# Kernel tuning notes

Measured on AMD Instinct MI355X. Metric: run time of the kernel, lower is better.

The kernel has to match this reference:

```python
import jax, jax.numpy as jnp
import numpy as np

B, K, D, LS, NL = 32, 64, 256, 128, 2


def _xavier(key, shape):
    # torch xavier_uniform for Linear weight [out, in]
    fan_out, fan_in = shape[-2], shape[-1]
    lim = float(np.sqrt(6.0 / (fan_in + fan_out)))
    return jax.random.uniform(key, shape, jnp.float32, -lim, lim)


def setup_inputs():
    key = jax.random.key(0)
    ks = jax.random.split(key, 32)
    inp = {
        "X": jax.random.normal(ks[0], (B, K, D), jnp.float32),
        # per-layer stacked params [NL, ...]
        "k_w": _xavier(ks[1], (NL, D, D)),
        "q_w": _xavier(ks[2], (NL, D, D)),
        "rv_w1": _xavier(ks[3], (NL, D, 2 * D)),
        "rv_b1": jnp.zeros((NL, D), jnp.float32),
        "rv_w2": _xavier(ks[4], (NL, D, D)),
        "rv_b2": jnp.zeros((NL, D), jnp.float32),
        "ln_g": jnp.ones((NL, D), jnp.float32),
        "ln_b": jnp.zeros((NL, D), jnp.float32),
        "mlp_w1": _xavier(ks[5], (NL, D, D)),
        "mlp_b1": jnp.zeros((NL, D), jnp.float32),
        "mlp_w2": _xavier(ks[6], (NL, D, D)),
        "mlp_b2": jnp.zeros((NL, D), jnp.float32),
        "proj_w": _xavier(ks[7], (LS, D)),
        "proj_b": jnp.zeros((LS,), jnp.float32),
        "mu_w": _xavier(ks[8], (LS, LS)),
        "mu_b": jnp.zeros((LS,), jnp.float32),
        "sp_w": _xavier(ks[9], (LS, LS)),
        "sp_b": jnp.zeros((LS,), jnp.float32),
    }
    return inp


def _gelu(x):
    return jax.nn.gelu(x, approximate=False)


def _layernorm(x, g, b, eps=1e-5):
    m = jnp.mean(x, axis=-1, keepdims=True)
    v = jnp.mean((x - m) ** 2, axis=-1, keepdims=True)
    return (x - m) / jnp.sqrt(v + eps) * g + b


def _block(x, kw, qw, rw1, rb1, rw2, rb2, lg, lb, mw1, mb1, mw2, mb2):
    scale = D ** (-0.5)
    x_orig = x
    # pairwise difference r[b,i,j,:] = x[b,i]-x[b,j]
    r = x[:, :, None, :] - x[:, None, :, :]                      # [B,K,K,D]
    xi = jnp.broadcast_to(x[:, :, None, :], (B, K, K, D))
    cat = jnp.concatenate([xi, r], axis=-1)                      # [B,K,K,2D]
    v = _gelu(jnp.einsum('bijc,dc->bijd', cat, rw1) + rb1)
    v = jnp.einsum('bijd,ed->bije', v, rw2) + rb2                # [B,K,K,D]
    k = jnp.einsum('bid,ed->bie', x, kw)
    q = jnp.einsum('bid,ed->bie', x, qw) * scale
    attn = jax.nn.softmax(jnp.einsum('bid,bjd->bij', q, k), axis=2)
    agg = jnp.einsum('bij,bijd->bid', attn, v)
    h = _layernorm(x_orig + agg, lg, lb)
    h = jnp.einsum('bid,ed->bie', _gelu(jnp.einsum('bid,ed->bie', h, mw1) + mb1), mw2) + mb2
    return x_orig + h


def reference(X, k_w, q_w, rv_w1, rv_b1, rv_w2, rv_b2, ln_g, ln_b,
              mlp_w1, mlp_b1, mlp_w2, mlp_b2, proj_w, proj_b,
              mu_w, mu_b, sp_w, sp_b):
    x = X
    for i in range(NL):
        x = _block(x, k_w[i], q_w[i], rv_w1[i], rv_b1[i], rv_w2[i], rv_b2[i],
                   ln_g[i], ln_b[i], mlp_w1[i], mlp_b1[i], mlp_w2[i], mlp_b2[i])
    s = jnp.sum(x, axis=1)                                        # [B,D]
    h = _gelu(s @ proj_w.T + proj_b)                              # [B,LS]
    mu = h @ mu_w.T + mu_b
    scale = jax.nn.softplus(h @ sp_w.T + sp_b)
    return (mu, scale)
```

## Files before the change

### kernel.cpp

```cpp
#include <hip/hip_runtime.h>
#include <hip/hip_bf16.h>


using bf16 = __hip_bfloat16;
typedef short bf16x8 __attribute__((ext_vector_type(8)));
typedef float f32x4 __attribute__((ext_vector_type(4)));

__device__ __forceinline__ float bfu(unsigned short u) { return __uint_as_float(((unsigned)u) << 16); }

__device__ __forceinline__ unsigned short bfr(float v) {
  unsigned u = __float_as_uint(v);
  u += 0x7FFFu + ((u >> 16) & 1u);
  return (unsigned short)(u >> 16);
}

__device__ __forceinline__ float gelu_e(float x) {
  return 0.5f * x * (1.0f + erff(x * 0.7071067811865475f));
}

__device__ __forceinline__ float load_f(const void* p, int i, int fl) {
  if (fl) return bfu(((const unsigned short*)p)[i]);
  return ((const float*)p)[i];
}

__device__ __forceinline__ int block_detect(const void* X) {
  __shared__ int bad_s;
  if (threadIdx.x == 0) bad_s = 0;
  __syncthreads();
  if (threadIdx.x < 256) {
    const float v = bfu(((const unsigned short*)X)[threadIdx.x]);
    if (!(fabsf(v) < 1e6f)) atomicOr(&bad_s, 1);
  }
  __syncthreads();
  return bad_s ? 0 : 1;
}

__device__ __forceinline__ void stage_split4(unsigned short (&aF)[2][4096], int row, int d0, float4 v) {
  ushort4 h, lo;
  h.x = bfr(v.x); h.y = bfr(v.y); h.z = bfr(v.z); h.w = bfr(v.w);
  lo.x = bfr(v.x - bfu(h.x)); lo.y = bfr(v.y - bfu(h.y));
  lo.z = bfr(v.z - bfu(h.z)); lo.w = bfr(v.w - bfu(h.w));
  const int kt = d0 >> 5, lane = row | (((d0 >> 3) & 3) << 4), j = d0 & 7;
  *(ushort4*)&aF[0][kt*512 + lane*8 + j] = h;
  *(ushort4*)&aF[1][kt*512 + lane*8 + j] = lo;
}

__global__ __launch_bounds__(256) void prep_kernel(
    const void* __restrict__ X, const void* __restrict__ kw, const void* __restrict__ qw,
    const void* __restrict__ rw1, const void* __restrict__ rw2, const void* __restrict__ mw1,
    const void* __restrict__ mw2, const void* __restrict__ pw, const void* __restrict__ muw,
    const void* __restrict__ spw,
    const void* __restrict__ rb1, const void* __restrict__ rb2, const void* __restrict__ lng,
    const void* __restrict__ lnb, const void* __restrict__ mb1, const void* __restrict__ mb2,
    const void* __restrict__ pb, const void* __restrict__ mub, const void* __restrict__ spb,
    unsigned short* __restrict__ wfb, unsigned short* __restrict__ w3b,
    float* __restrict__ wh, float* __restrict__ bc)
{
  __shared__ __align__(16) char psm[65536];
  const int fl = block_detect(X);
  const int t = threadIdx.x;
  int blk = blockIdx.x;

  if (blk < 16) {
    unsigned short* ls = (unsigned short*)psm;
    unsigned* lsu = (unsigned*)psm;
    const int l = blk >> 3, kt = blk & 7;
    if (fl) {
      #pragma unroll
      for (int s = 0; s < 4; ++s) {
        const unsigned* sp = (const unsigned*)((s == 0) ? kw : (s == 1) ? qw : rw1);
        const int rstr = (s < 2) ? 128 : 256;
        const int coff = ((s == 3) ? 128 : 0) + kt*16;
        for (int i = t; i < 4096; i += 256) {
          const int e = i >> 4, d2 = i & 15;
          lsu[s*4096 + i] = sp[(l*256 + e)*rstr + coff + d2];
        }
      }
    } else {
      #pragma unroll
      for (int s = 0; s < 4; ++s) {
        const float* sp = (const float*)((s == 0) ? kw : (s == 1) ? qw : rw1);
        const int rstr = (s < 2) ? 256 : 512;
        const int coff = ((s == 3) ? 256 : 0) + kt*32;
        for (int i = t; i < 4096; i += 256) {
          const int e = i >> 4, d2 = i & 15;
          const float f0 = sp[(l*256 + e)*rstr + coff + d2*2];
          const float f1 = sp[(l*256 + e)*rstr + coff + d2*2 + 1];
          lsu[s*4096 + i] = (unsigned)bfr(f0) | ((unsigned)bfr(f1) << 16);
        }
      }
    }
    __syncthreads();
    unsigned* outp = (unsigned*)wfb + (l*8 + kt)*16384;
    for (int f2 = t; f2 < 16384; f2 += 256) {
      const int j2 = f2 & 3, lane = (f2 >> 2) & 63, ntg = f2 >> 8;
      const int seg = ntg >> 4;
      const int e = (ntg & 15)*16 + (lane & 15);
      const int dl = ((lane >> 4) & 3)*8 + j2*2;
      unsigned short r0 = ls[seg*8192 + e*32 + dl];
      unsigned short r1 = ls[seg*8192 + e*32 + dl + 1];
      if (seg == 1) { r0 = bfr(bfu(r0)*0.0625f); r1 = bfr(bfu(r1)*0.0625f); }
      else if (seg == 2) {
        const unsigned short w0 = ls[3*8192 + e*32 + dl];
        const unsigned short w1 = ls[3*8192 + e*32 + dl + 1];
        r0 = bfr(bfu(r0) + bfu(w0)); r1 = bfr(bfu(r1) + bfu(w1));
      }
      outp[f2] = (unsigned)r0 | ((unsigned)r1 << 16);
    }
    return;
  }
  blk -= 16;
  if (blk < 48) {
    unsigned short* ls = (unsigned short*)psm;
    unsigned* lsu = (unsigned*)psm;
    const int l3 = blk >> 3, kt = blk & 7;
    const int l = l3 / 3, gm = l3 % 3;
    const void* src = (gm == 0) ? rw2 : (gm == 1) ? mw1 : mw2;
    if (fl) {
      const unsigned* sp = (const unsigned*)src;
      for (int i = t; i < 4096; i += 256) {
        const int e = i >> 4, d2 = i & 15;
        lsu[i] = sp[(l*256 + e)*128 + kt*16 + d2];
      }
    } else {
      const float* sp = (const float*)src;
      for (int i = t; i < 4096; i += 256) {
        const int e = i >> 4, d2 = i & 15;
        const float f0 = sp[(l*256 + e)*256 + kt*32 + d2*2];
        const float f1 = sp[(l*256 + e)*256 + kt*32 + d2*2 + 1];
        lsu[i] = (unsigned)bfr(f0) | ((unsigned)bfr(f1) << 16);
      }
    }
    __syncthreads();
    unsigned* outp = (unsigned*)w3b + (l3*8 + kt)*4096;
    for (int f2 = t; f2 < 4096; f2 += 256) {
      const int j2 = f2 & 3, lane = (f2 >> 2) & 63, nt = f2 >> 8;
      const int e = nt*16 + (lane & 15);
      const int dl = ((lane >> 4) & 3)*8 + j2*2;
      outp[f2] = (unsigned)ls[e*32 + dl] | ((unsigned)ls[e*32 + dl + 1] << 16);
    }
    return;
  }
  blk -= 48;
  if (blk < 24) {
    float* lsf = (float*)psm;
    if (blk < 8) {
      const int l0 = blk*16;
      if (fl) {
        const unsigned* sp = (const unsigned*)pw;
        for (int i = t; i < 2048; i += 256) {
          const int ll = i >> 7, d2 = i & 127;
          const unsigned u = sp[(l0 + ll)*128 + d2];
          lsf[ll*256 + d2*2]     = __uint_as_float(u << 16);
          lsf[ll*256 + d2*2 + 1] = __uint_as_float(u & 0xffff0000u);
        }
      } else {
        const float* sp = (const float*)pw;
        for (int i = t; i < 4096; i += 256) {
          const int ll = i >> 8, d = i & 255;
          lsf[ll*256 + d] = sp[(l0 + ll)*256 + d];
        }
      }
      __syncthreads();
      for (int i = t; i < 4096; i += 256) {
        const int d = i >> 4, ll = i & 15;
        wh[d*128 + l0 + ll] = lsf[ll*256 + d];
      }
    } else {
      const int grp2 = blk - 8;
      const int isSp = grp2 >> 3;
      const int l0 = (grp2 & 7)*16;
      const void* src = isSp ? spw : muw;
      const int off = isSp ? 49152 : 32768;
      if (fl) {
        const unsigned* sp = (const unsigned*)src;
        for (int i = t; i < 1024; i += 256) {
          const int ll = i >> 6, c2 = i & 63;
          const unsigned u = sp[(l0 + ll)*64 + c2];
          lsf[ll*128 + c2*2]     = __uint_as_float(u << 16);
          lsf[ll*128 + c2*2 + 1] = __uint_as_float(u & 0xffff0000u);
        }
      } else {
        const float* sp = (const float*)src;
        for (int i = t; i < 2048; i += 256) {
          const int ll = i >> 7, c = i & 127;
          lsf[ll*128 + c] = sp[(l0 + ll)*128 + c];
        }
      }
      __syncthreads();
      for (int i = t; i < 2048; i += 256) {
        const int c = i >> 4, ll = i & 15;
        wh[off + c*128 + l0 + ll] = lsf[ll*128 + c];
      }
    }
    return;
  }
  for (int i = t; i < 3456; i += 256) {
    const void* src; int off;
    if (i < 512)       { src = rb1; off = i; }
    else if (i < 1024) { src = rb2; off = i - 512; }
    else if (i < 1536) { src = lng; off = i - 1024; }
    else if (i < 2048) { src = lnb; off = i - 1536; }
    else if (i < 2560) { src = mb1; off = i - 2048; }
    else if (i < 3072) { src = mb2; off = i - 2560; }
    else if (i < 3200) { src = pb;  off = i - 3072; }
    else if (i < 3328) { src = mub; off = i - 3200; }
    else               { src = spb; off = i - 3328; }
    bc[i] = load_f(src, off, fl);
  }
}

template<bool SPLIT, int NTG>
__device__ __forceinline__ void k1_body(
    const unsigned short (&aF)[2][4096],
    const unsigned short* __restrict__ wfb, const float* __restrict__ bc,
    float* __restrict__ kq, float* __restrict__ Pf, unsigned* __restrict__ Qpk,
    int l, int row0, int ntg0, int t)
{
  const int w = t >> 6, l64 = t & 63;
  const int col = l64 & 15, quad = l64 >> 4;
  f32x4 acc[NTG];
  #pragma unroll
  for (int i = 0; i < NTG; ++i) acc[i] = (f32x4){0.f, 0.f, 0.f, 0.f};
  for (int kt = 0; kt < 8; ++kt) {
    const bf16x8 ah = *(const bf16x8*)&aF[0][kt*512 + l64*8];
    bf16x8 al;
    if (SPLIT) al = *(const bf16x8*)&aF[1][kt*512 + l64*8];
    #pragma unroll
    for (int i = 0; i < NTG; ++i) {
      const int ntg = ntg0 + w*NTG + i;
      const bf16x8 b = *(const bf16x8*)&wfb[((l*8 + kt)*64 + ntg)*512 + l64*8];
      acc[i] = __builtin_amdgcn_mfma_f32_16x16x32_bf16(ah, b, acc[i], 0, 0, 0);
      if (SPLIT) acc[i] = __builtin_amdgcn_mfma_f32_16x16x32_bf16(al, b, acc[i], 0, 0, 0);
    }
  }
  #pragma unroll
  for (int i = 0; i < NTG; ++i) {
    const int ntg = ntg0 + w*NTG + i;
    if (ntg < 32) {
      const int n = ntg*16 + col;
      #pragma unroll
      for (int r = 0; r < 4; ++r)
        kq[(size_t)(row0 + quad*4 + r)*512 + n] = acc[i][r];
    } else if (ntg < 48) {
      const int c = (ntg - 32)*16 + col;
      const float bias = bc[l*256 + c];
      #pragma unroll
      for (int r = 0; r < 4; ++r)
        Pf[(size_t)(row0 + quad*4 + r)*256 + c] = acc[i][r] + bias;
    } else {
      #pragma unroll
      for (int r = 0; r < 4; ++r) {
        const float v = acc[i][r];
        const float pv = __shfl_xor(v, 1, 64);
        if (!(col & 1)) {
          const unsigned uu = (unsigned)bfr(v) | ((unsigned)bfr(pv) << 16);
          Qpk[(size_t)(row0 + quad*4 + r)*128 + (ntg - 48)*8 + (col >> 1)] = uu;
        }
      }
    }
  }
}

template<bool SPLIT, int NRR>
__device__ __forceinline__ void k1_body16(
    const unsigned short (&aF)[2][4096],
    const unsigned short* __restrict__ wfb, const float* __restrict__ bc,
    float* __restrict__ kq, float* __restrict__ Pf, unsigned* __restrict__ Qpk,
    int l, int row0, int t)
{
  const int w = t >> 6, l64 = t & 63;
  const int col = l64 & 15, quad = l64 >> 4;
  f32x4 acc[4];
  #pragma unroll
  for (int i = 0; i < 4; ++i) acc[i] = (f32x4){0.f, 0.f, 0.f, 0.f};
  for (int kt = 0; kt < 8; ++kt) {
    const bf16x8 ah = *(const bf16x8*)&aF[0][kt*512 + l64*8];
    bf16x8 al;
    if (SPLIT) al = *(const bf16x8*)&aF[1][kt*512 + l64*8];
    #pragma unroll
    for (int i = 0; i < 4; ++i) {
      const int ntg = w*4 + i;
      const bf16x8 b = *(const bf16x8*)&wfb[((l*8 + kt)*64 + ntg)*512 + l64*8];
      acc[i] = __builtin_amdgcn_mfma_f32_16x16x32_bf16(ah, b, acc[i], 0, 0, 0);
      if (SPLIT) acc[i] = __builtin_amdgcn_mfma_f32_16x16x32_bf16(al, b, acc[i], 0, 0, 0);
    }
  }
  #pragma unroll
  for (int i = 0; i < 4; ++i) {
    const int ntg = w*4 + i;
    if (ntg < 32) {
      const int n = ntg*16 + col;
      #pragma unroll
      for (int r = 0; r < 4; ++r)
        if (NRR == 16 || quad*4 + r < NRR)
          kq[(size_t)(row0 + quad*4 + r)*512 + n] = acc[i][r];
    } else if (ntg < 48) {
      const int c = (ntg - 32)*16 + col;
      const float bias = bc[l*256 + c];
      #pragma unroll
      for (int r = 0; r < 4; ++r)
        if (NRR == 16 || quad*4 + r < NRR)
          Pf[(size_t)(row0 + quad*4 + r)*256 + c] = acc[i][r] + bias;
    } else {
      #pragma unroll
      for (int r = 0; r < 4; ++r) {
        const float v = acc[i][r];
        const float pv = __shfl_xor(v, 1, 64);
        if (!(col & 1) && (NRR == 16 || quad*4 + r < NRR)) {
          const unsigned uu = (unsigned)bfr(v) | ((unsigned)bfr(pv) << 16);
          Qpk[(size_t)(row0 + quad*4 + r)*128 + (ntg - 48)*8 + (col >> 1)] = uu;
        }
      }
    }
  }
}

__global__ __launch_bounds__(256) void k1l0(
    const void* __restrict__ X, const unsigned short* __restrict__ wfb,
    const float* __restrict__ bc, float* __restrict__ kq, float* __restrict__ Pf,
    unsigned* __restrict__ Qpk)
{
  const int fl = block_detect(X);
  __shared__ __align__(16) unsigned short aF[2][4096];
  const int t = threadIdx.x;
  const int mb = (int)blockIdx.x >> 2, nb4 = (int)blockIdx.x & 3;
  const int row0 = mb * 16, ntg0 = nb4 * 16;
  if (fl) {
    for (int i = t; i < 512; i += 256) {
      const int row = i >> 5, d0 = (i & 31) * 8;
      const uint4 u = *(const uint4*)((const unsigned*)X + (size_t)(row0 + row)*128 + (i & 31)*4);
      const int kt = d0 >> 5, lane = row | (((d0 >> 3) & 3) << 4);
      *(uint4*)&aF[0][kt*512 + lane*8] = u;
    }
  } else {
    for (int i = t; i < 1024; i += 256) {
      const int row = i >> 6, d0 = (i & 63) * 4;
      stage_split4(aF, row, d0, *(const float4*)((const float*)X + (size_t)(row0 + row)*256 + d0));
    }
  }
  __syncthreads();
  if (fl) k1_body<false, 4>(aF, wfb, bc, kq, Pf, Qpk, 0, row0, ntg0, t);
  else    k1_body<true,  4>(aF, wfb, bc, kq, Pf, Qpk, 0, row0, ntg0, t);
}

template<int NR>
__device__ __forceinline__ void attn_phase1k(
    const float* __restrict__ kq, const float* __restrict__ Pf,
    const unsigned* __restrict__ Qpk,
    int row0, int t, float* qg, float* scp, float* als,
    unsigned* Kst, unsigned* Qst)
{
  const int base = row0 & ~63;
  for (int i = t; i < NR*64; i += 1024) {
    const int il = i >> 6, d0 = (i & 63)*4;
    *(float4*)&qg[il*256 + d0] = *(const float4*)&kq[(size_t)(row0 + il)*512 + 256 + d0];
  }
  for (int i = t; i < 4096; i += 1024) {
    const int row = i >> 6, c4 = i & 63;
    const float4 v = *(const float4*)&kq[(size_t)(base + row)*512 + c4*4];
    Kst[row*132 + c4*2]     = (unsigned)bfr(v.x) | ((unsigned)bfr(v.y) << 16);
    Kst[row*132 + c4*2 + 1] = (unsigned)bfr(v.z) | ((unsigned)bfr(v.w) << 16);
  }
  for (int i = t; i < 2048; i += 1024) {
    const int row = i >> 5, c4 = i & 31;
    *(uint4*)&Qst[row*128 + c4*4] = *(const uint4*)&Qpk[(size_t)(base + row)*128 + c4*4];
  }
  __syncthreads();
  const int w = t >> 6, lane = t & 63;
  {
    const int jl = lane & 15, part = lane >> 4;
    const int j = (w & 3)*16 + jl;
    const int i0 = (w >> 2) * 2;
    const unsigned* kr = &Kst[j*132 + part*32];
    const float* q0p = &qg[i0*256 + part*64];
    const float* q1p = &qg[(i0+1)*256 + part*64];
    float s0 = 0.f, s1 = 0.f;
    #pragma unroll
    for (int d2 = 0; d2 < 32; d2 += 2) {
      const unsigned ka = kr[d2], kb = kr[d2 + 1];
      const float4 q0 = *(const float4*)&q0p[d2*2];
      const float4 q1 = *(const float4*)&q1p[d2*2];
      const float k0 = bfu((unsigned short)ka), k1 = bfu((unsigned short)(ka >> 16));
      const float k2 = bfu((unsigned short)kb), k3 = bfu((unsigned short)(kb >> 16));
      s0 = fmaf(k0, q0.x, s0); s0 = fmaf(k1, q0.y, s0);
      s0 = fmaf(k2, q0.z, s0); s0 = fmaf(k3, q0.w, s0);
      s1 = fmaf(k0, q1.x, s1); s1 = fmaf(k1, q1.y, s1);
      s1 = fmaf(k2, q1.z, s1); s1 = fmaf(k3, q1.w, s1);
    }
    s0 += __shfl_xor(s0, 16, 64); s0 += __shfl_xor(s0, 32, 64);
    s1 += __shfl_xor(s1, 16, 64); s1 += __shfl_xor(s1, 32, 64);
    if (part == 0) { scp[i0*64 + j] = s0; scp[(i0+1)*64 + j] = s1; }
  }
  __syncthreads();
  if (w < NR) {
    const int r = w;
    float s = scp[r*64 + lane];
    float m = s;
    #pragma unroll
    for (int off = 32; off; off >>= 1) m = fmaxf(m, __shfl_xor(m, off, 64));
    const float e = __expf(s - m);
    float ss = e;
    #pragma unroll
    for (int off = 32; off; off >>= 1) ss += __shfl_xor(ss, off, 64);
    als[r*64 + lane] = e / ss;
  }
  __syncthreads();
  {
    const int cp = t & 127, rb = t >> 7;
    const float2 P = *(const float2*)&Pf[(size_t)(row0 + rb)*256 + cp*2];
    const float A0 = -1.702f * P.x, A1 = -1.702f * P.y;
    float a0 = 0.f, a1 = 0.f;
    const unsigned* qp = &Qst[cp];
    const float* ap = &als[rb*64];
    #pragma unroll 4
    for (int j = 0; j < 64; ++j) {
      const unsigned u = qp[j*128];
      const float wgt = ap[j];
      const float q0 = __uint_as_float(u << 16);
      const float q1 = __uint_as_float(u & 0xffff0000u);
      const float s0 = __builtin_amdgcn_rcpf(1.f + __expf(fmaf(1.702f, q0, A0)));
      const float s1 = __builtin_amdgcn_rcpf(1.f + __expf(fmaf(1.702f, q1, A1)));
      a0 = fmaf(wgt * (P.x - q0), s0, a0);
      a1 = fmaf(wgt * (P.y - q1), s1, a1);
    }
    qg[rb*256 + cp*2]     = a0;
    qg[rb*256 + cp*2 + 1] = a1;
  }
  __syncthreads();
}

__device__ __forceinline__ f32x4 k4_gemm16(
    const unsigned short (&aF)[2][4096],
    const unsigned short* __restrict__ wg, int w, int l64)
{
  f32x4 acc = (f32x4){0.f, 0.f, 0.f, 0.f};
  for (int kt = 0; kt < 8; ++kt) {
    const bf16x8 ah = *(const bf16x8*)&aF[0][kt*512 + l64*8];
    const bf16x8 al = *(const bf16x8*)&aF[1][kt*512 + l64*8];
    const bf16x8 b = *(const bf16x8*)&wg[((kt*16 + w)*64 + l64)*8];
    acc = __builtin_amdgcn_mfma_f32_16x16x32_bf16(ah, b, acc, 0, 0, 0);
    acc = __builtin_amdgcn_mfma_f32_16x16x32_bf16(al, b, acc, 0, 0, 0);
  }
  return acc;
}

template<bool ADAPT, bool TAIL, int NR>
__device__ __forceinline__ void k4_core1k(
    const float* gl, const void* __restrict__ xin, int fl,
    float* __restrict__ xout, const unsigned short* __restrict__ wg,
    const float* __restrict__ bc, int l, int row0, int t, bool writeX,
    unsigned short (&aF)[2][4096], float* bufB, float (&mv)[16][2])
{
  const int w = t >> 6, l64 = t & 63;
  const int col = l64 & 15, quad = l64 >> 4;
  const int cn = w*16 + col;
  const float* rb2c = bc + 512  + l*256;
  const float* lngc = bc + 1024 + l*256;
  const float* lnbc = bc + 1536 + l*256;
  const float* mb1c = bc + 2048 + l*256;
  const float* mb2c = bc + 2560 + l*256;

  for (int i = t; i < NR*64; i += 1024) {
    const int row = i >> 6, d0 = (i & 63) * 4;
    stage_split4(aF, row, d0, *(const float4*)&gl[row*256 + d0]);
  }
  if (ADAPT && fl) {
    for (int c = t; c < NR*128; c += 1024) {
      const int row = c >> 7, dp = c & 127;
      const unsigned u = ((const unsigned*)xin)[(size_t)(row0 + row)*128 + dp];
      bufB[row*260 + dp*2]     = __uint_as_float(u << 16);
      bufB[row*260 + dp*2 + 1] = __uint_as_float(u & 0xffff0000u);
    }
  } else {
    for (int c = t; c < NR*64; c += 1024) {
      const int row = c >> 6, d0 = (c & 63) * 4;
      *(float4*)&bufB[row*260 + d0] = *(const float4*)((const float*)xin + (size_t)(row0 + row)*256 + d0);
    }
  }
  __syncthreads();
  float xtr[4];
  #pragma unroll
  for (int r = 0; r < 4; ++r) xtr[r] = bufB[(quad*4 + r)*260 + cn];
  __syncthreads();

  f32x4 acc = k4_gemm16(aF, wg, w, l64);
  #pragma unroll
  for (int r = 0; r < 4; ++r)
    bufB[(quad*4 + r)*260 + cn] = acc[r] + rb2c[cn] + xtr[r];
  __syncthreads();
  {
    const int row = t >> 5, part = t & 31;
    if (row < NR) {
      float s = 0.f, s2 = 0.f;
      #pragma unroll
      for (int kk = 0; kk < 8; ++kk) {
        const float v = bufB[row*260 + part + kk*32];
        s += v; s2 = fmaf(v, v, s2);
      }
      #pragma unroll
      for (int off = 16; off; off >>= 1) {
        s  += __shfl_xor(s, off, 32);
        s2 += __shfl_xor(s2, off, 32);
      }
      if (part == 0) {
        const float mu = s * (1.f/256.f);
        mv[row][0] = mu;
        mv[row][1] = rsqrtf(fmaf(-mu, mu, s2 * (1.f/256.f)) + 1e-5f);
      }
    }
  }
  __syncthreads();
  for (int i = t; i < NR*64; i += 1024) {
    const int row = i >> 6, d0 = (i & 63) * 4;
    float4 v = *(const float4*)&bufB[row*260 + d0];
    const float m = mv[row][0], iv = mv[row][1];
    v.x = (v.x - m)*iv*lngc[d0]   + lnbc[d0];
    v.y = (v.y - m)*iv*lngc[d0+1] + lnbc[d0+1];
    v.z = (v.z - m)*iv*lngc[d0+2] + lnbc[d0+2];
    v.w = (v.w - m)*iv*lngc[d0+3] + lnbc[d0+3];
    stage_split4(aF, row, d0, v);
  }
  __syncthreads();
  acc = k4_gemm16(aF, wg + 65536, w, l64);
  #pragma unroll
  for (int r = 0; r < 4; ++r)
    if (quad*4 + r < NR)
      bufB[(quad*4 + r)*260 + cn] = gelu_e(acc[r] + mb1c[cn]);
  __syncthreads();
  for (int i = t; i < NR*64; i += 1024) {
    const int row = i >> 6, d0 = (i & 63) * 4;
    stage_split4(aF, row, d0, *(const float4*)&bufB[row*260 + d0]);
  }
  __syncthreads();
  acc = k4_gemm16(aF, wg + 2*65536, w, l64);
  if (TAIL) {
    #pragma unroll
    for (int r = 0; r < 4; ++r)
      bufB[(quad*4 + r)*260 + cn] = acc[r] + mb2c[cn] + xtr[r];
    __syncthreads();
    for (int i = t; i < NR*64; i += 1024) {
      const int row = i >> 6, d0 = (i & 63) * 4;
      const float4 v = *(const float4*)&bufB[row*260 + d0];
      if (writeX) *(float4*)&xout[(size_t)(row0 + row)*256 + d0] = v;
      stage_split4(aF, row, d0, v);
    }
    __syncthreads();
  } else {
    #pragma unroll
    for (int r = 0; r < 4; ++r)
      if (quad*4 + r < NR)
        xout[(size_t)(row0 + quad*4 + r)*256 + cn] = acc[r] + mb2c[cn] + xtr[r];
  }
}

#define SM_QG    0
#define SM_SCP   8192
#define SM_ALS   10240
#define SM_UNION 12288
#define SM_QST   46080
#define SM_AF    12288
#define SM_BUFB  28672
#define SM_MV    45312
#define SM_TOTAL 78848

__device__ __forceinline__ int swz_row0(int bid) {
  const int xcd = bid & 7, j = bid >> 3;
  const int batch = (j & 3)*8 + xcd;
  const int rsub = j >> 2;
  return batch*64 + rsub*8;
}

__global__ __launch_bounds__(1024) void kA_attn_mix_kq(
    const unsigned short* __restrict__ w3b, const unsigned short* __restrict__ wfb,
    const float* __restrict__ bc, const void* __restrict__ X, float* __restrict__ x,
    const float* __restrict__ kq, const float* __restrict__ Pf,
    const unsigned* __restrict__ Qpk,
    float* __restrict__ kq1, float* __restrict__ Pf1, unsigned* __restrict__ Qpk1)
{
  const int fl = block_detect(X);
  __shared__ __align__(16) char sm[SM_TOTAL];
  float* qg  = (float*)(sm + SM_QG);
  float* scp = (float*)(sm + SM_SCP);
  float* als = (float*)(sm + SM_ALS);
  unsigned* Kst = (unsigned*)(sm + SM_UNION);
  unsigned* Qst = (unsigned*)(sm + SM_QST);
  unsigned short (&aF)[2][4096] = *reinterpret_cast<unsigned short (*)[2][4096]>(sm + SM_AF);
  float* bufB = (float*)(sm + SM_BUFB);
  float (&mv)[16][2] = *reinterpret_cast<float (*)[16][2]>(sm + SM_MV);
  const int t = threadIdx.x;
  const int row0 = swz_row0((int)blockIdx.x);
  attn_phase1k<8>(kq, Pf, Qpk, row0, t, qg, scp, als, Kst, Qst);
  k4_core1k<true, true, 8>(qg, X, fl, x, w3b, bc, 0, row0, t, true, aF, bufB, mv);
  k1_body16<true, 8>(aF, wfb, bc, kq1, Pf1, Qpk1, 1, row0, t);
}

__global__ __launch_bounds__(1024) void kB_attn_fin(
    const unsigned short* __restrict__ w3b, const float* __restrict__ bc,
    float* __restrict__ x, const float* __restrict__ kq1,
    const float* __restrict__ Pf1, const unsigned* __restrict__ Qpk1)
{
  __shared__ __align__(16) char sm[SM_TOTAL];
  float* qg  = (float*)(sm + SM_QG);
  float* scp = (float*)(sm + SM_SCP);
  float* als = (float*)(sm + SM_ALS);
  unsigned* Kst = (unsigned*)(sm + SM_UNION);
  unsigned* Qst = (unsigned*)(sm + SM_QST);
  unsigned short (&aF)[2][4096] = *reinterpret_cast<unsigned short (*)[2][4096]>(sm + SM_AF);
  float* bufB = (float*)(sm + SM_BUFB);
  float (&mv)[16][2] = *reinterpret_cast<float (*)[16][2]>(sm + SM_MV);
  const int t = threadIdx.x;
  const int row0 = swz_row0((int)blockIdx.x);
  attn_phase1k<8>(kq1, Pf1, Qpk1, row0, t, qg, scp, als, Kst, Qst);
  k4_core1k<false, false, 8>(qg, x, 0, x, w3b + 3*65536, bc, 1, row0, t, true, aF, bufB, mv);
}

__global__ __launch_bounds__(256) void k5_head(
    const float* __restrict__ x, const float* __restrict__ wh,
    const float* __restrict__ bc, const void* __restrict__ X,
    void* __restrict__ out)
{
  const int fl = block_detect(X);
  __shared__ float ss[256];
  __shared__ float hh[128];
  const int b = blockIdx.x, t = threadIdx.x;
  {
    const float* xp = x + (size_t)(b << 6)*256 + t;
    float s0 = 0.f, s1 = 0.f, s2 = 0.f, s3 = 0.f;
    for (int i = 0; i < 64; i += 4) {
      s0 += xp[(size_t)(i    )*256];
      s1 += xp[(size_t)(i + 1)*256];
      s2 += xp[(size_t)(i + 2)*256];
      s3 += xp[(size_t)(i + 3)*256];
    }
    ss[t] = (s0 + s1) + (s2 + s3);
  }
  __syncthreads();
  if (t < 128) {
    float acc = bc[3072 + t];
    const float* projT = wh;
    for (int d = 0; d < 256; ++d) acc = fmaf(ss[d], projT[d*128 + t], acc);
    hh[t] = gelu_e(acc);
  }
  __syncthreads();
  float v; int oidx;
  if (t < 128) {
    float acc = bc[3200 + t];
    const float* muT = wh + 32768;
    for (int c = 0; c < 128; ++c) acc = fmaf(hh[c], muT[c*128 + t], acc);
    v = acc; oidx = b*128 + t;
  } else {
    const int u = t - 128;
    float acc = bc[3328 + u];
    const float* spT = wh + 49152;
    for (int c = 0; c < 128; ++c) acc = fmaf(hh[c], spT[c*128 + u], acc);
    v = (acc > 20.f) ? acc : log1pf(__expf(acc));
    oidx = 4096 + b*128 + u;
  }
  if (fl) ((bf16*)out)[oidx] = __float2bfloat16(v);
  else    ((float*)out)[oidx] = v;
}

extern "C" void kernel_launch(void* const* d_in, const int* in_sizes, int n_in,
                              void* d_out, int out_size, void* d_ws, size_t ws_size,
                              hipStream_t stream)
{
  (void)in_sizes; (void)n_in; (void)out_size; (void)ws_size;
  float* ws    = (float*)d_ws;
  float* x     = ws + 16;
  float* kq    = x + 524288;
  float* Pf    = kq + 1048576;
  unsigned* Qpk = (unsigned*)(Pf + 524288);
  float* g     = (float*)(Qpk + 262144);
  unsigned short* wfb = (unsigned short*)(g + 524288);
  unsigned short* w3b = wfb + 524288;
  float* wh    = (float*)(w3b + 393216);
  float* bc    = wh + 65536;
  float* kq1   = bc + 4096;
  float* Pf1   = kq1 + 1048576;
  unsigned* Qpk1 = (unsigned*)(Pf1 + 524288);

  prep_kernel<<<dim3(89), dim3(256), 0, stream>>>(
      d_in[0], d_in[1], d_in[2], d_in[3], d_in[5], d_in[9], d_in[11],
      d_in[13], d_in[15], d_in[17],
      d_in[4], d_in[6], d_in[7], d_in[8], d_in[10], d_in[12],
      d_in[14], d_in[16], d_in[18],
      wfb, w3b, wh, bc);
  k1l0<<<dim3(512), dim3(256), 0, stream>>>(d_in[0], wfb, bc, kq, Pf, Qpk);
  kA_attn_mix_kq<<<dim3(256), dim3(1024), 0, stream>>>(
      w3b, wfb, bc, d_in[0], x, kq, Pf, Qpk, kq1, Pf1, Qpk1);
  kB_attn_fin<<<dim3(256), dim3(1024), 0, stream>>>(w3b, bc, x, kq1, Pf1, Qpk1);
  k5_head<<<dim3(32), dim3(256), 0, stream>>>(x, wh, bc, d_in[0], (void*)d_out);
}
```

Before: 187.2 us.

## Fuse attention kernels and head into one kernel with per-batch atomic barriers

Merges the layer-0 attention/mix kernel, the layer-1 attention kernel and the head kernel into a single launch. Blocks of the same batch synchronise through a spin-wait counter in workspace, and the last block to finish each batch (found with an atomic ticket) runs the head. The head's reductions are also split across 1024 threads. This removes two kernel launches and their gaps, at the cost of relying on all 8 blocks of a batch being co-resident for the spin barrier, plus spin and fence overhead.

Result: slower. 432.2 us (+130.9%).

```diff
diff --git a/kernel.cpp b/kernel.cpp
--- a/kernel.cpp
+++ b/kernel.cpp
@@ -54,7 +54,7 @@
     const void* __restrict__ lnb, const void* __restrict__ mb1, const void* __restrict__ mb2,
     const void* __restrict__ pb, const void* __restrict__ mub, const void* __restrict__ spb,
     unsigned short* __restrict__ wfb, unsigned short* __restrict__ w3b,
-    float* __restrict__ wh, float* __restrict__ bc)
+    float* __restrict__ wh, float* __restrict__ bc, unsigned* __restrict__ cnt)
 {
   __shared__ __align__(16) char psm[65536];
   const int fl = block_detect(X);
@@ -195,6 +195,7 @@
     }
     return;
   }
+  for (int i = t; i < 64; i += 256) cnt[i] = 0u;
   for (int i = t; i < 3456; i += 256) {
     const void* src; int off;
     if (i < 512)       { src = rb1; off = i; }
@@ -571,15 +572,18 @@
   return batch*64 + rsub*8;
 }
 
-__global__ __launch_bounds__(1024) void kA_attn_mix_kq(
+__global__ __launch_bounds__(1024) void kABh(
     const unsigned short* __restrict__ w3b, const unsigned short* __restrict__ wfb,
     const float* __restrict__ bc, const void* __restrict__ X, float* __restrict__ x,
     const float* __restrict__ kq, const float* __restrict__ Pf,
     const unsigned* __restrict__ Qpk,
-    float* __restrict__ kq1, float* __restrict__ Pf1, unsigned* __restrict__ Qpk1)
+    float* __restrict__ kq1, float* __restrict__ Pf1, unsigned* __restrict__ Qpk1,
+    const float* __restrict__ wh, void* __restrict__ out,
+    unsigned* __restrict__ cnt1, unsigned* __restrict__ cnt2)
 {
   const int fl = block_detect(X);
   __shared__ __align__(16) char sm[SM_TOTAL];
+  __shared__ unsigned rank_s;
   float* qg  = (float*)(sm + SM_QG);
   float* scp = (float*)(sm + SM_SCP);
   float* als = (float*)(sm + SM_ALS);
@@ -590,75 +594,87 @@
   float (&mv)[16][2] = *reinterpret_cast<float (*)[16][2]>(sm + SM_MV);
   const int t = threadIdx.x;
   const int row0 = swz_row0((int)blockIdx.x);
+  const int batch = row0 >> 6;
+
   attn_phase1k<8>(kq, Pf, Qpk, row0, t, qg, scp, als, Kst, Qst);
   k4_core1k<true, true, 8>(qg, X, fl, x, w3b, bc, 0, row0, t, true, aF, bufB, mv);
   k1_body16<true, 8>(aF, wfb, bc, kq1, Pf1, Qpk1, 1, row0, t);
-}
-
-__global__ __launch_bounds__(1024) void kB_attn_fin(
-    const unsigned short* __restrict__ w3b, const float* __restrict__ bc,
-    float* __restrict__ x, const float* __restrict__ kq1,
-    const float* __restrict__ Pf1, const unsigned* __restrict__ Qpk1)
-{
-  __shared__ __align__(16) char sm[SM_TOTAL];
-  float* qg  = (float*)(sm + SM_QG);
-  float* scp = (float*)(sm + SM_SCP);
-  float* als = (float*)(sm + SM_ALS);
-  unsigned* Kst = (unsigned*)(sm + SM_UNION);
-  unsigned* Qst = (unsigned*)(sm + SM_QST);
-  unsigned short (&aF)[2][4096] = *reinterpret_cast<unsigned short (*)[2][4096]>(sm + SM_AF);
-  float* bufB = (float*)(sm + SM_BUFB);
-  float (&mv)[16][2] = *reinterpret_cast<float (*)[16][2]>(sm + SM_MV);
-  const int t = threadIdx.x;
-  const int row0 = swz_row0((int)blockIdx.x);
+
+  __threadfence();
+  __syncthreads();
+  if (t == 0) {
+    __hip_atomic_fetch_add(&cnt1[batch], 1u, __ATOMIC_RELEASE, __HIP_MEMORY_SCOPE_AGENT);
+    while (__hip_atomic_load(&cnt1[batch], __ATOMIC_ACQUIRE, __HIP_MEMORY_SCOPE_AGENT) < 8u)
+      __builtin_amdgcn_s_sleep(4);
+  }
+  __syncthreads();
+  __threadfence();
+
   attn_phase1k<8>(kq1, Pf1, Qpk1, row0, t, qg, scp, als, Kst, Qst);
   k4_core1k<false, false, 8>(qg, x, 0, x, w3b + 3*65536, bc, 1, row0, t, true, aF, bufB, mv);
-}
-
-__global__ __launch_bounds__(256) void k5_head(
-    const float* __restrict__ x, const float* __restrict__ wh,
-    const float* __restrict__ bc, const void* __restrict__ X,
-    void* __restrict__ out)
-{
-  const int fl = block_detect(X);
-  __shared__ float ss[256];
-  __shared__ float hh[128];
-  const int b = blockIdx.x, t = threadIdx.x;
+
+  __threadfence();
+  __syncthreads();
+  if (t == 0)
+    rank_s = __hip_atomic_fetch_add(&cnt2[batch], 1u, __ATOMIC_ACQ_REL, __HIP_MEMORY_SCOPE_AGENT);
+  __syncthreads();
+  if (rank_s != 7u) return;
+  __threadfence();
+
+  float* ss4 = (float*)(sm);
+  float* ssf = (float*)(sm + 4096);
+  float* hh  = (float*)(sm + 5120);
+  float* red = (float*)(sm + 8192);
   {
-    const float* xp = x + (size_t)(b << 6)*256 + t;
+    const int col = t & 255, q = t >> 8;
+    const float* xp = x + (size_t)(batch*64 + q*16)*256 + col;
     float s0 = 0.f, s1 = 0.f, s2 = 0.f, s3 = 0.f;
-    for (int i = 0; i < 64; i += 4) {
+    for (int i = 0; i < 16; i += 4) {
       s0 += xp[(size_t)(i    )*256];
       s1 += xp[(size_t)(i + 1)*256];
       s2 += xp[(size_t)(i + 2)*256];
       s3 += xp[(size_t)(i + 3)*256];
     }
-    ss[t] = (s0 + s1) + (s2 + s3);
+    ss4[q*256 + col] = (s0 + s1) + (s2 + s3);
+  }
+  __syncthreads();
+  if (t < 256) ssf[t] = (ss4[t] + ss4[256 + t]) + (ss4[512 + t] + ss4[768 + t]);
+  __syncthreads();
+  {
+    const int o = t & 127, ch = t >> 7;
+    float acc = 0.f;
+    #pragma unroll 4
+    for (int d = ch*32; d < ch*32 + 32; ++d) acc = fmaf(ssf[d], wh[d*128 + o], acc);
+    red[t] = acc;
   }
   __syncthreads();
   if (t < 128) {
-    float acc = bc[3072 + t];
-    const float* projT = wh;
-    for (int d = 0; d < 256; ++d) acc = fmaf(ss[d], projT[d*128 + t], acc);
-    hh[t] = gelu_e(acc);
-  }
-  __syncthreads();
-  float v; int oidx;
-  if (t < 128) {
-    float acc = bc[3200 + t];
-    const float* muT = wh + 32768;
-    for (int c = 0; c < 128; ++c) acc = fmaf(hh[c], muT[c*128 + t], acc);
-    v = acc; oidx = b*128 + t;
-  } else {
-    const int u = t - 128;
-    float acc = bc[3328 + u];
-    const float* spT = wh + 49152;
-    for (int c = 0; c < 128; ++c) acc = fmaf(hh[c], spT[c*128 + u], acc);
-    v = (acc > 20.f) ? acc : log1pf(__expf(acc));
-    oidx = 4096 + b*128 + u;
-  }
-  if (fl) ((bf16*)out)[oidx] = __float2bfloat16(v);
-  else    ((float*)out)[oidx] = v;
+    float a = bc[3072 + t];
+    #pragma unroll
+    for (int ch = 0; ch < 8; ++ch) a += red[t + ch*128];
+    hh[t] = gelu_e(a);
+  }
+  __syncthreads();
+  {
+    const int o2 = t & 255, ch = t >> 8;
+    const int isSp = o2 >> 7, o = o2 & 127;
+    const float* W = wh + (isSp ? 49152 : 32768);
+    float acc = 0.f;
+    #pragma unroll 4
+    for (int c = ch*32; c < ch*32 + 32; ++c) acc = fmaf(hh[c], W[c*128 + o], acc);
+    red[t] = acc;
+  }
+  __syncthreads();
+  if (t < 256) {
+    const int isSp = t >> 7, o = t & 127;
+    const float a = ((red[t] + red[t + 256]) + (red[t + 512] + red[t + 768]))
+                    + bc[(isSp ? 3328 : 3200) + o];
+    float v; int oidx;
+    if (isSp == 0) { v = a; oidx = batch*128 + o; }
+    else { v = (a > 20.f) ? a : log1pf(__expf(a)); oidx = 4096 + batch*128 + o; }
+    if (fl) ((bf16*)out)[oidx] = __float2bfloat16(v);
+    else    ((float*)out)[oidx] = v;
+  }
 }
 
 extern "C" void kernel_launch(void* const* d_in, const int* in_sizes, int n_in,
@@ -667,7 +683,8 @@
 {
   (void)in_sizes; (void)n_in; (void)out_size; (void)ws_size;
   float* ws    = (float*)d_ws;
-  float* x     = ws + 16;
+  unsigned* cnt = (unsigned*)ws;
+  float* x     = ws + 128;
   float* kq    = x + 524288;
   float* Pf    = kq + 1048576;
   unsigned* Qpk = (unsigned*)(Pf + 524288);
@@ -685,10 +702,9 @@
       d_in[13], d_in[15], d_in[17],
       d_in[4], d_in[6], d_in[7], d_in[8], d_in[10], d_in[12],
       d_in[14], d_in[16], d_in[18],
-      wfb, w3b, wh, bc);
+      wfb, w3b, wh, bc, cnt);
   k1l0<<<dim3(512), dim3(256), 0, stream>>>(d_in[0], wfb, bc, kq, Pf, Qpk);
-  kA_attn_mix_kq<<<dim3(256), dim3(1024), 0, stream>>>(
-      w3b, wfb, bc, d_in[0], x, kq, Pf, Qpk, kq1, Pf1, Qpk1);
-  kB_attn_fin<<<dim3(256), dim3(1024), 0, stream>>>(w3b, bc, x, kq1, Pf1, Qpk1);
-  k5_head<<<dim3(32), dim3(256), 0, stream>>>(x, wh, bc, d_in[0], (void*)d_out);
-}
+  kABh<<<dim3(256), dim3(1024), 0, stream>>>(
+      w3b, wfb, bc, d_in[0], x, kq, Pf, Qpk, kq1, Pf1, Qpk1,
+      wh, (void*)d_out, cnt, cnt + 32);
+}
```

## Halve rows per attention block to double grid size and re-split layer-0 projection

Applied to the files above, without the earlier changes.

The two fused attention kernels now give each block 4 query rows instead of 8 and launch 512 blocks instead of 256, so the GPU's CUs get more blocks to spread across. The per-row score, softmax and relation-aggregation loops are simplified to one output per thread to match. The layer-0 projection kernel now uses 512-thread blocks that cover 8 rows and 32 column tiles each, and both projection paths share one generic body. The cost is that every block re-stages the full 64-row K and Q tiles for fewer rows, and half of each 16-row MFMA tile is wasted. The new launch-bound occupancy hints may also limit registers and cause spills.

Result: slower. 195.7 us (+4.5%).

```diff
diff --git a/kernel.cpp b/kernel.cpp
--- a/kernel.cpp
+++ b/kernel.cpp
@@ -210,64 +210,12 @@
   }
 }
 
-template<bool SPLIT, int NTG>
-__device__ __forceinline__ void k1_body(
+template<bool SPLIT, int NRR>
+__device__ __forceinline__ void k1_bodyN(
     const unsigned short (&aF)[2][4096],
     const unsigned short* __restrict__ wfb, const float* __restrict__ bc,
     float* __restrict__ kq, float* __restrict__ Pf, unsigned* __restrict__ Qpk,
     int l, int row0, int ntg0, int t)
-{
-  const int w = t >> 6, l64 = t & 63;
-  const int col = l64 & 15, quad = l64 >> 4;
-  f32x4 acc[NTG];
-  #pragma unroll
-  for (int i = 0; i < NTG; ++i) acc[i] = (f32x4){0.f, 0.f, 0.f, 0.f};
-  for (int kt = 0; kt < 8; ++kt) {
-    const bf16x8 ah = *(const bf16x8*)&aF[0][kt*512 + l64*8];
-    bf16x8 al;
-    if (SPLIT) al = *(const bf16x8*)&aF[1][kt*512 + l64*8];
-    #pragma unroll
-    for (int i = 0; i < NTG; ++i) {
-      const int ntg = ntg0 + w*NTG + i;
-      const bf16x8 b = *(const bf16x8*)&wfb[((l*8 + kt)*64 + ntg)*512 + l64*8];
-      acc[i] = __builtin_amdgcn_mfma_f32_16x16x32_bf16(ah, b, acc[i], 0, 0, 0);
-      if (SPLIT) acc[i] = __builtin_amdgcn_mfma_f32_16x16x32_bf16(al, b, acc[i], 0, 0, 0);
-    }
-  }
-  #pragma unroll
-  for (int i = 0; i < NTG; ++i) {
-    const int ntg = ntg0 + w*NTG + i;
-    if (ntg < 32) {
-      const int n = ntg*16 + col;
-      #pragma unroll
-      for (int r = 0; r < 4; ++r)
-        kq[(size_t)(row0 + quad*4 + r)*512 + n] = acc[i][r];
-    } else if (ntg < 48) {
-      const int c = (ntg - 32)*16 + col;
-      const float bias = bc[l*256 + c];
-      #pragma unroll
-      for (int r = 0; r < 4; ++r)
-        Pf[(size_t)(row0 + quad*4 + r)*256 + c] = acc[i][r] + bias;
-    } else {
-      #pragma unroll
-      for (int r = 0; r < 4; ++r) {
-        const float v = acc[i][r];
-        const float pv = __shfl_xor(v, 1, 64);
-        if (!(col & 1)) {
-          const unsigned uu = (unsigned)bfr(v) | ((unsigned)bfr(pv) << 16);
-          Qpk[(size_t)(row0 + quad*4 + r)*128 + (ntg - 48)*8 + (col >> 1)] = uu;
-        }
-      }
-    }
-  }
-}
-
-template<bool SPLIT, int NRR>
-__device__ __forceinline__ void k1_body16(
-    const unsigned short (&aF)[2][4096],
-    const unsigned short* __restrict__ wfb, const float* __restrict__ bc,
-    float* __restrict__ kq, float* __restrict__ Pf, unsigned* __restrict__ Qpk,
-    int l, int row0, int t)
 {
   const int w = t >> 6, l64 = t & 63;
   const int col = l64 & 15, quad = l64 >> 4;
@@ -280,7 +228,7 @@
     if (SPLIT) al = *(const bf16x8*)&aF[1][kt*512 + l64*8];
     #pragma unroll
     for (int i = 0; i < 4; ++i) {
-      const int ntg = w*4 + i;
+      const int ntg = ntg0 + w*4 + i;
       const bf16x8 b = *(const bf16x8*)&wfb[((l*8 + kt)*64 + ntg)*512 + l64*8];
       acc[i] = __builtin_amdgcn_mfma_f32_16x16x32_bf16(ah, b, acc[i], 0, 0, 0);
       if (SPLIT) acc[i] = __builtin_amdgcn_mfma_f32_16x16x32_bf16(al, b, acc[i], 0, 0, 0);
@@ -288,7 +236,7 @@
   }
   #pragma unroll
   for (int i = 0; i < 4; ++i) {
-    const int ntg = w*4 + i;
+    const int ntg = ntg0 + w*4 + i;
     if (ntg < 32) {
       const int n = ntg*16 + col;
       #pragma unroll
@@ -316,7 +264,7 @@
   }
 }
 
-__global__ __launch_bounds__(256) void k1l0(
+__global__ __launch_bounds__(512, 4) void k1l0(
     const void* __restrict__ X, const unsigned short* __restrict__ wfb,
     const float* __restrict__ bc, float* __restrict__ kq, float* __restrict__ Pf,
     unsigned* __restrict__ Qpk)
@@ -324,35 +272,34 @@
   const int fl = block_detect(X);
   __shared__ __align__(16) unsigned short aF[2][4096];
   const int t = threadIdx.x;
-  const int mb = (int)blockIdx.x >> 2, nb4 = (int)blockIdx.x & 3;
-  const int row0 = mb * 16, ntg0 = nb4 * 16;
+  const int row0 = ((int)blockIdx.x >> 1) * 8;
+  const int ntg0 = ((int)blockIdx.x & 1) * 32;
   if (fl) {
-    for (int i = t; i < 512; i += 256) {
+    for (int i = t; i < 256; i += 512) {
       const int row = i >> 5, d0 = (i & 31) * 8;
       const uint4 u = *(const uint4*)((const unsigned*)X + (size_t)(row0 + row)*128 + (i & 31)*4);
       const int kt = d0 >> 5, lane = row | (((d0 >> 3) & 3) << 4);
       *(uint4*)&aF[0][kt*512 + lane*8] = u;
     }
   } else {
-    for (int i = t; i < 1024; i += 256) {
+    for (int i = t; i < 512; i += 512) {
       const int row = i >> 6, d0 = (i & 63) * 4;
       stage_split4(aF, row, d0, *(const float4*)((const float*)X + (size_t)(row0 + row)*256 + d0));
     }
   }
   __syncthreads();
-  if (fl) k1_body<false, 4>(aF, wfb, bc, kq, Pf, Qpk, 0, row0, ntg0, t);
-  else    k1_body<true,  4>(aF, wfb, bc, kq, Pf, Qpk, 0, row0, ntg0, t);
-}
-
-template<int NR>
-__device__ __forceinline__ void attn_phase1k(
+  if (fl) k1_bodyN<false, 8>(aF, wfb, bc, kq, Pf, Qpk, 0, row0, ntg0, t);
+  else    k1_bodyN<true,  8>(aF, wfb, bc, kq, Pf, Qpk, 0, row0, ntg0, t);
+}
+
+__device__ __forceinline__ void attn_phase4(
     const float* __restrict__ kq, const float* __restrict__ Pf,
     const unsigned* __restrict__ Qpk,
     int row0, int t, float* qg, float* scp, float* als,
     unsigned* Kst, unsigned* Qst)
 {
   const int base = row0 & ~63;
-  for (int i = t; i < NR*64; i += 1024) {
+  for (int i = t; i < 256; i += 1024) {
     const int il = i >> 6, d0 = (i & 63)*4;
     *(float4*)&qg[il*256 + d0] = *(const float4*)&kq[(size_t)(row0 + il)*512 + 256 + d0];
   }
@@ -371,31 +318,25 @@
   {
     const int jl = lane & 15, part = lane >> 4;
     const int j = (w & 3)*16 + jl;
-    const int i0 = (w >> 2) * 2;
+    const int i0 = w >> 2;
     const unsigned* kr = &Kst[j*132 + part*32];
-    const float* q0p = &qg[i0*256 + part*64];
-    const float* q1p = &qg[(i0+1)*256 + part*64];
-    float s0 = 0.f, s1 = 0.f;
+    const float* qp = &qg[i0*256 + part*64];
+    float s0 = 0.f;
     #pragma unroll
     for (int d2 = 0; d2 < 32; d2 += 2) {
       const unsigned ka = kr[d2], kb = kr[d2 + 1];
-      const float4 q0 = *(const float4*)&q0p[d2*2];
-      const float4 q1 = *(const float4*)&q1p[d2*2];
-      const float k0 = bfu((unsigned short)ka), k1 = bfu((unsigned short)(ka >> 16));
-      const float k2 = bfu((unsigned short)kb), k3 = bfu((unsigned short)(kb >> 16));
-      s0 = fmaf(k0, q0.x, s0); s0 = fmaf(k1, q0.y, s0);
-      s0 = fmaf(k2, q0.z, s0); s0 = fmaf(k3, q0.w, s0);
-      s1 = fmaf(k0, q1.x, s1); s1 = fmaf(k1, q1.y, s1);
-      s1 = fmaf(k2, q1.z, s1); s1 = fmaf(k3, q1.w, s1);
+      const float4 q0 = *(const float4*)&qp[d2*2];
+      s0 = fmaf(bfu((unsigned short)ka),         q0.x, s0);
+      s0 = fmaf(bfu((unsigned short)(ka >> 16)), q0.y, s0);
+      s0 = fmaf(bfu((unsigned short)kb),         q0.z, s0);
+      s0 = fmaf(bfu((unsigned short)(kb >> 16)), q0.w, s0);
     }
     s0 += __shfl_xor(s0, 16, 64); s0 += __shfl_xor(s0, 32, 64);
-    s1 += __shfl_xor(s1, 16, 64); s1 += __shfl_xor(s1, 32, 64);
-    if (part == 0) { scp[i0*64 + j] = s0; scp[(i0+1)*64 + j] = s1; }
-  }
-  __syncthreads();
-  if (w < NR) {
-    const int r = w;
-    float s = scp[r*64 + lane];
+    if (part == 0) scp[i0*64 + j] = s0;
+  }
+  __syncthreads();
+  if (w < 4) {
+    float s = scp[w*64 + lane];
     float m = s;
     #pragma unroll
     for (int off = 32; off; off >>= 1) m = fmaxf(m, __shfl_xor(m, off, 64));
@@ -403,29 +344,25 @@
     float ss = e;
     #pragma unroll
     for (int off = 32; off; off >>= 1) ss += __shfl_xor(ss, off, 64);
-    als[r*64 + lane] = e / ss;
+    als[w*64 + lane] = e / ss;
   }
   __syncthreads();
   {
-    const int cp = t & 127, rb = t >> 7;
-    const float2 P = *(const float2*)&Pf[(size_t)(row0 + rb)*256 + cp*2];
-    const float A0 = -1.702f * P.x, A1 = -1.702f * P.y;
-    float a0 = 0.f, a1 = 0.f;
-    const unsigned* qp = &Qst[cp];
+    const int c = t & 255, rb = t >> 8;
+    const float P = Pf[(size_t)(row0 + rb)*256 + c];
+    const float A0 = -1.702f * P;
+    float a0 = 0.f;
+    const unsigned* qp = &Qst[c >> 1];
+    const bool hi = (c & 1);
     const float* ap = &als[rb*64];
     #pragma unroll 4
     for (int j = 0; j < 64; ++j) {
       const unsigned u = qp[j*128];
-      const float wgt = ap[j];
-      const float q0 = __uint_as_float(u << 16);
-      const float q1 = __uint_as_float(u & 0xffff0000u);
-      const float s0 = __builtin_amdgcn_rcpf(1.f + __expf(fmaf(1.702f, q0, A0)));
-      const float s1 = __builtin_amdgcn_rcpf(1.f + __expf(fmaf(1.702f, q1, A1)));
-      a0 = fmaf(wgt * (P.x - q0), s0, a0);
-      a1 = fmaf(wgt * (P.y - q1), s1, a1);
-    }
-    qg[rb*256 + cp*2]     = a0;
-    qg[rb*256 + cp*2 + 1] = a1;
+      const float q = hi ? __uint_as_float(u & 0xffff0000u) : __uint_as_float(u << 16);
+      const float s = __builtin_amdgcn_rcpf(1.f + __expf(fmaf(1.702f, q, A0)));
+      a0 = fmaf(ap[j] * (P - q), s, a0);
+    }
+    qg[rb*256 + c] = a0;
   }
   __syncthreads();
 }
@@ -564,14 +501,14 @@
 #define SM_MV    45312
 #define SM_TOTAL 78848
 
-__device__ __forceinline__ int swz_row0(int bid) {
+__device__ __forceinline__ int swz_row0_512(int bid) {
   const int xcd = bid & 7, j = bid >> 3;
   const int batch = (j & 3)*8 + xcd;
   const int rsub = j >> 2;
-  return batch*64 + rsub*8;
-}
-
-__global__ __launch_bounds__(1024) void kA_attn_mix_kq(
+  return batch*64 + rsub*4;
+}
+
+__global__ __launch_bounds__(1024, 8) void kA_attn_mix_kq(
     const unsigned short* __restrict__ w3b, const unsigned short* __restrict__ wfb,
     const float* __restrict__ bc, const void* __restrict__ X, float* __restrict__ x,
     const float* __restrict__ kq, const float* __restrict__ Pf,
@@ -589,13 +526,13 @@
   float* bufB = (float*)(sm + SM_BUFB);
   float (&mv)[16][2] = *reinterpret_cast<float (*)[16][2]>(sm + SM_MV);
   const int t = threadIdx.x;
-  const int row0 = swz_row0((int)blockIdx.x);
-  attn_phase1k<8>(kq, Pf, Qpk, row0, t, qg, scp, als, Kst, Qst);
-  k4_core1k<true, true, 8>(qg, X, fl, x, w3b, bc, 0, row0, t, true, aF, bufB, mv);
-  k1_body16<true, 8>(aF, wfb, bc, kq1, Pf1, Qpk1, 1, row0, t);
-}
-
-__global__ __launch_bounds__(1024) void kB_attn_fin(
+  const int row0 = swz_row0_512((int)blockIdx.x);
+  attn_phase4(kq, Pf, Qpk, row0, t, qg, scp, als, Kst, Qst);
+  k4_core1k<true, true, 4>(qg, X, fl, x, w3b, bc, 0, row0, t, true, aF, bufB, mv);
+  k1_bodyN<true, 4>(aF, wfb, bc, kq1, Pf1, Qpk1, 1, row0, 0, t);
+}
+
+__global__ __launch_bounds__(1024, 8) void kB_attn_fin(
     const unsigned short* __restrict__ w3b, const float* __restrict__ bc,
     float* __restrict__ x, const float* __restrict__ kq1,
     const float* __restrict__ Pf1, const unsigned* __restrict__ Qpk1)
@@ -610,9 +547,9 @@
   float* bufB = (float*)(sm + SM_BUFB);
   float (&mv)[16][2] = *reinterpret_cast<float (*)[16][2]>(sm + SM_MV);
   const int t = threadIdx.x;
-  const int row0 = swz_row0((int)blockIdx.x);
-  attn_phase1k<8>(kq1, Pf1, Qpk1, row0, t, qg, scp, als, Kst, Qst);
-  k4_core1k<false, false, 8>(qg, x, 0, x, w3b + 3*65536, bc, 1, row0, t, true, aF, bufB, mv);
+  const int row0 = swz_row0_512((int)blockIdx.x);
+  attn_phase4(kq1, Pf1, Qpk1, row0, t, qg, scp, als, Kst, Qst);
+  k4_core1k<false, false, 4>(qg, x, 0, x, w3b + 3*65536, bc, 1, row0, t, true, aF, bufB, mv);
 }
 
 __global__ __launch_bounds__(256) void k5_head(
@@ -686,9 +623,9 @@
       d_in[4], d_in[6], d_in[7], d_in[8], d_in[10], d_in[12],
       d_in[14], d_in[16], d_in[18],
       wfb, w3b, wh, bc);
-  k1l0<<<dim3(512), dim3(256), 0, stream>>>(d_in[0], wfb, bc, kq, Pf, Qpk);
-  kA_attn_mix_kq<<<dim3(256), dim3(1024), 0, stream>>>(
+  k1l0<<<dim3(512), dim3(512), 0, stream>>>(d_in[0], wfb, bc, kq, Pf, Qpk);
+  kA_attn_mix_kq<<<dim3(512), dim3(1024), 0, stream>>>(
       w3b, wfb, bc, d_in[0], x, kq, Pf, Qpk, kq1, Pf1, Qpk1);
-  kB_attn_fin<<<dim3(256), dim3(1024), 0, stream>>>(w3b, bc, x, kq1, Pf1, Qpk1);
+  kB_attn_fin<<<dim3(512), dim3(1024), 0, stream>>>(w3b, bc, x, kq1, Pf1, Qpk1);
   k5_head<<<dim3(32), dim3(256), 0, stream>>>(x, wh, bc, d_in[0], (void*)d_out);
 }
```
